# Performance work log

Measured on AMD Instinct MI355X. Metric: run time of the kernel, lower is better.

Reference implementation:

```python
import jax, jax.numpy as jnp
import numpy as np

N_NODES = 20000
N_EDGES = 320000
EMB = 256
K_DIFF = 3
BN_EPS = 1e-5


def conv1d(x, w, b, stride):
    # x: [N, Cin, L], w: [Cout, Cin, K]
    y = jax.lax.conv_general_dilated(x, w, window_strides=(stride,), padding='VALID',
                                     dimension_numbers=('NCH', 'OIH', 'NCH'))
    return y + b[None, :, None]


def batchnorm_train(x, gamma, beta):
    # training-mode BatchNorm1d over (N, L) per channel, biased variance
    m = jnp.mean(x, axis=(0, 2), keepdims=True)
    v = jnp.var(x, axis=(0, 2), keepdims=True)
    return (x - m) * jax.lax.rsqrt(v + BN_EPS) * gamma[None, :, None] + beta[None, :, None]


def dconv(X, W, b, row, col, norm_out, norm_in, n):
    # Diffusion convolution (pytorch_geometric_temporal DConv), K hops,
    # forward (out-degree) and backward (in-degree) random walks.
    def prop(x, norm):
        msg = norm[:, None] * x[row]                    # [E, F] gather
        return jax.ops.segment_sum(msg, col, num_segments=n)  # scatter-add to targets

    K = W.shape[1]
    Tx_0 = X
    Tx_1 = X
    H = X @ W[0, 0] + X @ W[1, 0]
    if K > 1:
        Tx_1_o = prop(X, norm_out)
        Tx_1_i = prop(X, norm_in)
        H = H + Tx_1_o @ W[0, 1] + Tx_1_i @ W[1, 1]
    for k in range(2, K):
        Tx_2_o = 2.0 * prop(Tx_1_o, norm_out) - Tx_0
        Tx_2_i = 2.0 * prop(Tx_1_i, norm_in) - Tx_0
        H = H + Tx_2_o @ W[0, k] + Tx_2_i @ W[1, k]
        Tx_0, Tx_1_o, Tx_1_i = Tx_1, Tx_2_o, Tx_2_i
    return H + b


def setup_inputs() -> dict:
    key = jax.random.key(0)
    ks = jax.random.split(key, 16)
    d_in = 2 * EMB  # concat([X, H])
    inp = {
        'x': jax.random.normal(ks[0], (N_NODES, 1, 100), dtype=jnp.float32),
        'edge_index': jax.random.randint(ks[1], (2, N_EDGES), 0, N_NODES, dtype=jnp.int32),
        'hidden_state': jax.random.normal(ks[2], (N_NODES, EMB), dtype=jnp.float32),
        'conv1_w': jax.random.normal(ks[3], (32, 1, 10), dtype=jnp.float32) * 0.2,
        'conv1_b': jnp.zeros((32,), jnp.float32),
        'bn1_gamma': jnp.ones((32,), jnp.float32),
        'bn1_beta': jnp.zeros((32,), jnp.float32),
        'conv2_w': jax.random.normal(ks[4], (32, 32, 10), dtype=jnp.float32) * 0.05,
        'conv2_b': jnp.zeros((32,), jnp.float32),
        'bn2_gamma': jnp.ones((32,), jnp.float32),
        'bn2_beta': jnp.zeros((32,), jnp.float32),
        'W_z': jax.random.normal(ks[5], (2, K_DIFF, d_in, EMB), dtype=jnp.float32) * 0.05,
        'b_z': jnp.zeros((EMB,), jnp.float32),
        'W_r': jax.random.normal(ks[6], (2, K_DIFF, d_in, EMB), dtype=jnp.float32) * 0.05,
        'b_r': jnp.zeros((EMB,), jnp.float32),
        'W_h': jax.random.normal(ks[7], (2, K_DIFF, d_in, EMB), dtype=jnp.float32) * 0.05,
        'b_h': jnp.zeros((EMB,), jnp.float32),
    }
    return inp


def reference(x, edge_index, hidden_state, conv1_w, conv1_b, bn1_gamma, bn1_beta,
              conv2_w, conv2_b, bn2_gamma, bn2_beta, W_z, b_z, W_r, b_r, W_h, b_h):
    n = x.shape[0]
    # CNN embedding: conv -> relu -> bn, twice
    h = batchnorm_train(jax.nn.relu(conv1d(x, conv1_w, conv1_b, 3)), bn1_gamma, bn1_beta)
    h = batchnorm_train(jax.nn.relu(conv1d(h, conv2_w, conv2_b, 3)), bn2_gamma, bn2_beta)
    X = h.reshape(n, -1)  # [N, EMB]

    row, col = edge_index[0], edge_index[1]
    ones = jnp.ones((row.shape[0],), X.dtype)
    deg_out = jax.ops.segment_sum(ones, row, num_segments=n)
    deg_in = jax.ops.segment_sum(ones, col, num_segments=n)
    norm_out = (1.0 / deg_out)[row]
    norm_in = (1.0 / deg_in)[col]

    H0 = hidden_state
    XH = jnp.concatenate([X, H0], axis=1)
    Z = jax.nn.sigmoid(dconv(XH, W_z, b_z, row, col, norm_out, norm_in, n))
    R = jax.nn.sigmoid(dconv(XH, W_r, b_r, row, col, norm_out, norm_in, n))
    XRH = jnp.concatenate([X, R * H0], axis=1)
    H_tilde = jnp.tanh(dconv(XRH, W_h, b_h, row, col, norm_out, norm_in, n))
    H = Z * H0 + (1.0 - Z) * H_tilde
    return jax.nn.relu(H)
```

## Files before the change

### kernel.cpp

```cpp
#include <hip/hip_runtime.h>
#include <cstdint>
#include <cstddef>

#define NN 20000
#define NE 320000
#define SBUF 10240000

typedef float f32x4 __attribute__((ext_vector_type(4)));
typedef short s16x8 __attribute__((ext_vector_type(8)));
typedef unsigned short us;

__device__ __forceinline__ us f2bf(float x){
    unsigned u = __float_as_uint(x);
    unsigned r = (u + 0x7fffu + ((u >> 16) & 1u)) >> 16;
    return (us)r;
}
__device__ __forceinline__ float bf2f(us s){
    return __uint_as_float(((unsigned)s) << 16);
}

__device__ __forceinline__ void gl16(const void* g, void* l){
    __builtin_amdgcn_global_load_lds((const __attribute__((address_space(1))) unsigned int*)g,
                                     (__attribute__((address_space(3))) unsigned int*)l, 16, 0, 0);
}

__device__ __forceinline__ void upd8(uint4 v, float w, float* ao, float* ai){
    float f0=__uint_as_float(v.x<<16), f1=__uint_as_float(v.x&0xffff0000u);
    float f2=__uint_as_float(v.y<<16), f3=__uint_as_float(v.y&0xffff0000u);
    float f4=__uint_as_float(v.z<<16), f5=__uint_as_float(v.z&0xffff0000u);
    float f6=__uint_as_float(v.w<<16), f7=__uint_as_float(v.w&0xffff0000u);
    ao[0]=fmaf(w,f0,ao[0]); ao[1]=fmaf(w,f1,ao[1]); ao[2]=fmaf(w,f2,ao[2]); ao[3]=fmaf(w,f3,ao[3]);
    ao[4]=fmaf(w,f4,ao[4]); ao[5]=fmaf(w,f5,ao[5]); ao[6]=fmaf(w,f6,ao[6]); ao[7]=fmaf(w,f7,ao[7]);
    ai[0]+=f0; ai[1]+=f1; ai[2]+=f2; ai[3]+=f3; ai[4]+=f4; ai[5]+=f5; ai[6]+=f6; ai[7]+=f7;
}
__device__ __forceinline__ void updw(uint4 v, float w, float* a){
    float f0=__uint_as_float(v.x<<16), f1=__uint_as_float(v.x&0xffff0000u);
    float f2=__uint_as_float(v.y<<16), f3=__uint_as_float(v.y&0xffff0000u);
    float f4=__uint_as_float(v.z<<16), f5=__uint_as_float(v.z&0xffff0000u);
    float f6=__uint_as_float(v.w<<16), f7=__uint_as_float(v.w&0xffff0000u);
    a[0]=fmaf(w,f0,a[0]); a[1]=fmaf(w,f1,a[1]); a[2]=fmaf(w,f2,a[2]); a[3]=fmaf(w,f3,a[3]);
    a[4]=fmaf(w,f4,a[4]); a[5]=fmaf(w,f5,a[5]); a[6]=fmaf(w,f6,a[6]); a[7]=fmaf(w,f7,a[7]);
}
__device__ __forceinline__ uint4 pack8(const float* a){
    uint4 r;
    r.x=((unsigned)f2bf(a[1])<<16)|f2bf(a[0]);
    r.y=((unsigned)f2bf(a[3])<<16)|f2bf(a[2]);
    r.z=((unsigned)f2bf(a[5])<<16)|f2bf(a[4]);
    r.w=((unsigned)f2bf(a[7])<<16)|f2bf(a[6]);
    return r;
}
__device__ __forceinline__ uint4 pack8s(const float* a, float s){
    uint4 r;
    r.x=((unsigned)f2bf(s*a[1])<<16)|f2bf(s*a[0]);
    r.y=((unsigned)f2bf(s*a[3])<<16)|f2bf(s*a[2]);
    r.z=((unsigned)f2bf(s*a[5])<<16)|f2bf(s*a[4]);
    r.w=((unsigned)f2bf(s*a[7])<<16)|f2bf(s*a[6]);
    return r;
}


__global__ void k_zero(uint32_t* p, int n){
    int i = blockIdx.x*256 + threadIdx.x;
    if(i < n) p[i] = 0u;
}

__global__ void k_degree(const int* __restrict__ ei, int* degout, int* degin){
    int e = blockIdx.x*256 + threadIdx.x;
    if(e < NE){
        atomicAdd(&degout[ei[e]], 1);
        atomicAdd(&degin[ei[NE+e]], 1);
    }
}

__global__ void k_scan(const int* __restrict__ degin, int* __restrict__ coloff,
                       float* __restrict__ invdegin){
    __shared__ int part[1024];
    int t = threadIdx.x;
    int base = t*20;
    int s = 0;
    for(int k=0;k<20;k++){ int i = base+k; if(i < NN) s += degin[i]; }
    part[t] = s;
    __syncthreads();
    for(int off=1; off<1024; off<<=1){
        int v = (t>=off) ? part[t-off] : 0;
        __syncthreads();
        part[t] += v;
        __syncthreads();
    }
    int run = (t>0) ? part[t-1] : 0;
    for(int k=0;k<20;k++){
        int i = base+k;
        if(i < NN){
            int d = degin[i];
            coloff[i] = run;
            run += d;
            invdegin[i] = (d>0) ? (1.0f/(float)d) : 0.0f;
        }
    }
    if(t==1023) coloff[NN] = part[1023];
}

__global__ void k_csr(const int* __restrict__ ei, const int* __restrict__ degout,
                      const int* __restrict__ coloff, int* cnt, int2* __restrict__ ew){
    int e = blockIdx.x*256 + threadIdx.x;
    if(e < NE){
        int r = ei[e], c = ei[NE+e];
        int pos = coloff[c] + atomicAdd(&cnt[c], 1);
        int2 v; v.x = r; v.y = __float_as_int(1.0f/(float)degout[r]);
        ew[pos] = v;
    }
}


__global__ void k_conv1(const float* __restrict__ x, const float* __restrict__ w1,
                        const float* __restrict__ b1, us* __restrict__ y1T){
    __shared__ float w[320];
    __shared__ float bb[32];
    int t = threadIdx.x;
    for(int i=t;i<320;i+=256) w[i] = w1[i];
    if(t < 32) bb[t] = b1[t];
    __syncthreads();
    int gid = blockIdx.x*256 + t;
    int node = gid>>5, p = gid&31;
    us* yo = y1T + (size_t)node*1024 + p*32;
    if(p >= 31){
        uint4 z = {0,0,0,0};
        *(uint4*)yo = z; *(uint4*)(yo+8) = z;
        *(uint4*)(yo+16) = z; *(uint4*)(yo+24) = z;
        return;
    }
    const float* xr = x + node*100 + 3*p;
    float xv[10];
    #pragma unroll
    for(int k=0;k<10;k++) xv[k] = xr[k];
    float o[32];
    #pragma unroll
    for(int c=0;c<32;c++){
        float a = bb[c];
        #pragma unroll
        for(int k=0;k<10;k++) a = fmaf(w[c*10+k], xv[k], a);
        o[c] = fmaxf(a, 0.0f);
    }
    *(uint4*)yo      = pack8(o);
    *(uint4*)(yo+8)  = pack8(o+8);
    *(uint4*)(yo+16) = pack8(o+16);
    *(uint4*)(yo+24) = pack8(o+24);
}

__global__ void k_chanstats_T(const us* __restrict__ y, float* __restrict__ sq){
    int tid = blockIdx.x*256 + threadIdx.x;
    int slot = tid & 1023;
    int c = slot & 31;
    int node0 = tid >> 10;
    float s = 0.f, q = 0.f;
    for(int n=node0; n<NN; n+=64){
        float v = bf2f(y[(size_t)n*1024 + slot]);
        s += v; q = fmaf(v, v, q);
    }
    s += __shfl_xor(s, 32);
    q += __shfl_xor(q, 32);
    if((threadIdx.x & 63) < 32){
        atomicAdd(&sq[c], s);
        atomicAdd(&sq[32+c], q);
    }
}

template<int SLOTS, int PPC>
__global__ void k_chanstats_bf(const us* __restrict__ y, float* __restrict__ sq){
    int tid = blockIdx.x*blockDim.x + threadIdx.x;
    int slot = tid & (SLOTS-1);
    int node0 = tid / SLOTS;
    int nstride = (gridDim.x*blockDim.x) / SLOTS;
    int c = slot / PPC;
    float s = 0.f, q = 0.f;
    for(int n=node0; n<NN; n+=nstride){
        float v = bf2f(y[(size_t)n*SLOTS + slot]);
        s += v; q = fmaf(v, v, q);
    }
    #pragma unroll
    for(int m=PPC>>1; m>0; m>>=1){
        s += __shfl_xor(s, m);
        q += __shfl_xor(q, m);
    }
    if((threadIdx.x & (PPC-1)) == 0){
        atomicAdd(&sq[c], s);
        atomicAdd(&sq[32+c], q);
    }
}

__global__ void k_bnfin(const float* __restrict__ sq, const float* __restrict__ gamma,
                        const float* __restrict__ beta, float* __restrict__ scsh,
                        float inv_count){
    int c = threadIdx.x;
    if(c < 32){
        float m = sq[c]*inv_count;
        float v = sq[32+c]*inv_count - m*m;
        float sc = gamma[c]*rsqrtf(v + 1e-5f);
        scsh[c] = sc;
        scsh[32+c] = beta[c] - m*sc;
    }
}

__global__ void k_wfold(const float* __restrict__ w2, const float* __restrict__ scsh1,
                        us* __restrict__ Bf){
    int idx = blockIdx.x*256 + threadIdx.x;
    if(idx >= 10240) return;
    int kk = idx >> 10, c2 = (idx >> 5) & 31, c = idx & 31;
    Bf[idx] = f2bf(scsh1[c] * w2[c2*320 + c*10 + kk]);
}

__global__ void k_wbias(const float* __restrict__ w2, const float* __restrict__ scsh1,
                        const float* __restrict__ b2, float* __restrict__ biasc){
    int t = threadIdx.x;
    int c2 = t >> 3, part = t & 7;
    float s = 0.f;
    for(int i=part; i<320; i+=8)
        s += scsh1[32 + i/10] * w2[c2*320 + i];
    s += __shfl_xor(s,1); s += __shfl_xor(s,2); s += __shfl_xor(s,4);
    if(part == 0) biasc[c2] = b2[c2] + s;
}

__global__ void __launch_bounds__(256) k_conv2m(const us* __restrict__ y1T,
        const us* __restrict__ Bf, const float* __restrict__ biasc,
        us* __restrict__ Xpre){
    int t = threadIdx.x;
    int wv = t>>6, l = t&63;
    int l15 = l&15, g = l>>4;
    int r0 = blockIdx.x*64 + wv*16;
    int arow = r0 + l15;
    int an = arow>>3, ap = arow&7;
    const us* abase = y1T + (size_t)an*1024 + (3*ap)*32 + g*8;
    const us* bbase = Bf + (size_t)l15*32 + g*8;
    f32x4 acc0 = {}, acc1 = {};
    #pragma unroll
    for(int kk=0;kk<10;kk++){
        s16x8 af = *(const s16x8*)(abase + kk*32);
        s16x8 b0 = *(const s16x8*)(bbase + kk*1024);
        s16x8 b1 = *(const s16x8*)(bbase + kk*1024 + 512);
        acc0 = __builtin_amdgcn_mfma_f32_16x16x32_bf16(af, b0, acc0, 0, 0, 0);
        acc1 = __builtin_amdgcn_mfma_f32_16x16x32_bf16(af, b1, acc1, 0, 0, 0);
    }
    int base = r0 + g*4;
    int n = base>>3, p0 = base&7;
    #pragma unroll
    for(int nf=0;nf<2;nf++){
        int c2 = nf*16 + l15;
        float bb = biasc[c2];
        f32x4 a = nf ? acc1 : acc0;
        float v0 = fmaxf(a[0]+bb,0.f), v1 = fmaxf(a[1]+bb,0.f);
        float v2 = fmaxf(a[2]+bb,0.f), v3 = fmaxf(a[3]+bb,0.f);
        uint2 pk;
        pk.x = ((unsigned)f2bf(v1)<<16)|f2bf(v0);
        pk.y = ((unsigned)f2bf(v3)<<16)|f2bf(v2);
        *(uint2*)&Xpre[(size_t)n*256 + c2*8 + p0] = pk;
    }
}

__global__ void __launch_bounds__(256) k_prep(const us* __restrict__ Xpre,
        const float* __restrict__ scsh, const float* __restrict__ h0,
        us* __restrict__ XHp){
    int node = blockIdx.x*4 + (threadIdx.x>>6);
    if(node >= NN) return;
    int lane = threadIdx.x & 63;
    int half = lane>>5, g = lane&31;
    uint4 o;
    if(half == 0){
        uint4 v = *(const uint4*)(Xpre + (size_t)node*256 + g*8);
        float sc = scsh[g], sh = scsh[32+g];
        float y[8];
        y[0]=fmaf(sc,__uint_as_float(v.x<<16),sh); y[1]=fmaf(sc,__uint_as_float(v.x&0xffff0000u),sh);
        y[2]=fmaf(sc,__uint_as_float(v.y<<16),sh); y[3]=fmaf(sc,__uint_as_float(v.y&0xffff0000u),sh);
        y[4]=fmaf(sc,__uint_as_float(v.z<<16),sh); y[5]=fmaf(sc,__uint_as_float(v.z&0xffff0000u),sh);
        y[6]=fmaf(sc,__uint_as_float(v.w<<16),sh); y[7]=fmaf(sc,__uint_as_float(v.w&0xffff0000u),sh);
        o = pack8(y);
    }else{
        float4 a = *(const float4*)(h0 + (size_t)node*256 + g*8);
        float4 b = *(const float4*)(h0 + (size_t)node*256 + g*8 + 4);
        float y[8] = {a.x,a.y,a.z,a.w,b.x,b.y,b.z,b.w};
        o = pack8(y);
    }
    *(uint4*)(XHp + (size_t)node*512 + (size_t)g*16 + half*8) = o;
}


__device__ __forceinline__ float weff_val(const float* W, int term, size_t base){
    const size_t S = 512*256;
    if(term==0)      return W[0*S+base] + W[3*S+base] - W[2*S+base] - W[5*S+base];
    else if(term==1) return W[1*S+base];
    else if(term==2) return W[4*S+base];
    else if(term==3) return 2.0f*W[2*S+base];
    else             return 2.0f*W[5*S+base];
}

__global__ void k_weff_zr_t(const float* __restrict__ Wz, const float* __restrict__ Wr,
                            us* __restrict__ Wt){
    int k = blockIdx.x*256 + threadIdx.x;
    int col = blockIdx.y;
    const float* W = (col < 256) ? Wz : Wr;
    int j = col & 255;
    int kb = k >> 8, rr = k & 255;
    size_t base = (size_t)((kb & 1)*256 + rr)*256 + j;
    Wt[(size_t)col*2560 + k] = f2bf(weff_val(W, kb>>1, base));
}

__global__ void k_weff_h_t(const float* __restrict__ Wh, us* __restrict__ Wt){
    int k = blockIdx.x*256 + threadIdx.x;
    int col = blockIdx.y;
    int kb = k >> 8, rr = k & 255;
    size_t base = (size_t)((kb & 1)*256 + rr)*256 + col;
    Wt[(size_t)col*2560 + k] = f2bf(weff_val(Wh, kb>>1, base));
}


__global__ void __launch_bounds__(256) k_prop1(const us* __restrict__ XHp,
        const int* __restrict__ coloff, const int2* __restrict__ ew,
        const float* __restrict__ invdeg, us* __restrict__ T1op, us* __restrict__ T1ip){
    int node = blockIdx.x*4 + (threadIdx.x>>6);
    if(node >= NN) return;
    int lane = threadIdx.x & 63;
    size_t lo = (size_t)(lane&31)*16 + (lane>>5)*8;
    int s = __builtin_amdgcn_readfirstlane(coloff[node]);
    int e = __builtin_amdgcn_readfirstlane(coloff[node+1]);
    float ao[8]={0,0,0,0,0,0,0,0}, ai[8]={0,0,0,0,0,0,0,0};
    int j = s;
    for(; j+7 < e; j += 8){
        int2 ed[8]; uint4 v[8];
        #pragma unroll
        for(int i=0;i<8;i++) ed[i] = ew[j+i];
        #pragma unroll
        for(int i=0;i<8;i++) v[i] = *(const uint4*)(XHp+(size_t)ed[i].x*512+lo);
        #pragma unroll
        for(int i=0;i<8;i++) upd8(v[i], __int_as_float(ed[i].y), ao, ai);
    }
    for(; j < e; j++){
        int2 ed = ew[j];
        uint4 v = *(const uint4*)(XHp+(size_t)ed.x*512+lo);
        upd8(v, __int_as_float(ed.y), ao, ai);
    }
    float wi = invdeg[node];
    *(uint4*)(T1op+(size_t)node*512+lo) = pack8(ao);
    *(uint4*)(T1ip+(size_t)node*512+lo) = pack8s(ai,wi);
}

__global__ void __launch_bounds__(256) k_prop2(const us* __restrict__ T1op,
        const us* __restrict__ T1ip,
        const int* __restrict__ coloff, const int2* __restrict__ ew,
        const float* __restrict__ invdeg, us* __restrict__ P2op, us* __restrict__ P2ip){
    int node = blockIdx.x*4 + (threadIdx.x>>6);
    if(node >= NN) return;
    int lane = threadIdx.x & 63;
    size_t lo = (size_t)(lane&31)*16 + (lane>>5)*8;
    int s = __builtin_amdgcn_readfirstlane(coloff[node]);
    int e = __builtin_amdgcn_readfirstlane(coloff[node+1]);
    float ao[8]={0,0,0,0,0,0,0,0}, ai[8]={0,0,0,0,0,0,0,0};
    int j = s;
    for(; j+3 < e; j += 4){
        int2 ed[4]; uint4 va[4], vb[4];
        #pragma unroll
        for(int i=0;i<4;i++) ed[i] = ew[j+i];
        #pragma unroll
        for(int i=0;i<4;i++){
            size_t o = (size_t)ed[i].x*512+lo;
            va[i] = *(const uint4*)(T1op+o);
            vb[i] = *(const uint4*)(T1ip+o);
        }
        #pragma unroll
        for(int i=0;i<4;i++){
            updw(va[i], __int_as_float(ed[i].y), ao);
            updw(vb[i], 1.0f, ai);
        }
    }
    for(; j < e; j++){
        int2 ed = ew[j];
        size_t o = (size_t)ed.x*512+lo;
        updw(*(const uint4*)(T1op+o), __int_as_float(ed.y), ao);
        updw(*(const uint4*)(T1ip+o), 1.0f, ai);
    }
    float wi = invdeg[node];
    *(uint4*)(P2op+(size_t)node*512+lo) = pack8(ao);
    *(uint4*)(P2ip+(size_t)node*512+lo) = pack8s(ai,wi);
}

__global__ void __launch_bounds__(256) k_propu(const us* __restrict__ Yin,
        const int* __restrict__ coloff, const int2* __restrict__ ew,
        const float* __restrict__ invdeg, us* __restrict__ Pout){
    int node = blockIdx.x*4 + (threadIdx.x>>6);
    if(node >= NN) return;
    int lane = threadIdx.x & 63;
    int half = lane>>5;
    size_t lo = (size_t)(lane&31)*16 + half*8;
    int s = __builtin_amdgcn_readfirstlane(coloff[node]);
    int e = __builtin_amdgcn_readfirstlane(coloff[node+1]);
    float a[8]={0,0,0,0,0,0,0,0};
    int j = s;
    for(; j+7 < e; j += 8){
        int2 ed[8]; uint4 v[8];
        #pragma unroll
        for(int i=0;i<8;i++) ed[i] = ew[j+i];
        #pragma unroll
        for(int i=0;i<8;i++) v[i] = *(const uint4*)(Yin+(size_t)ed[i].x*512+lo);
        #pragma unroll
        for(int i=0;i<8;i++) updw(v[i], half ? 1.0f : __int_as_float(ed[i].y), a);
    }
    for(; j < e; j++){
        int2 ed = ew[j];
        uint4 v = *(const uint4*)(Yin+(size_t)ed.x*512+lo);
        updw(v, half ? 1.0f : __int_as_float(ed.y), a);
    }
    float sc = half ? invdeg[node] : 1.0f;
    *(uint4*)(Pout+(size_t)node*512+lo) = pack8s(a,sc);
}


template<int MODE, int BNT>
__global__ void __launch_bounds__(256) k_gemm(const us* __restrict__ XG,
        const us* __restrict__ RG, const us* __restrict__ Wt,
        const float* __restrict__ bias0, const float* __restrict__ bias1,
        const float* __restrict__ h0, const float* __restrict__ Zin,
        float* __restrict__ out0, us* __restrict__ out1){
    constexpr int WN = BNT/32;
    constexpr int NB = BNT/64;
    __shared__ us As[2][4096];
    __shared__ us Bs[2][BNT*32];
    int t = threadIdx.x;
    int wid = t >> 6, lane = t & 63;
    int l15 = lane & 15, kg = lane >> 4;

    int bid = blockIdx.x;
    int xcd = bid & 7, sblk = bid >> 3;
    int cidx = sblk & 3, r = (sblk >> 2)*8 + xcd;
    if(r >= 157) return;
    int row0 = r*128, col0 = cidx*BNT;
    int rowbase = (wid >> 1)*64, colbase = (wid & 1)*(BNT/2);
    int swz = (l15 >> 1) & 3;

    int srA[2], sgA[2];
    size_t rowoffA[2];
    #pragma unroll
    for(int i=0;i<2;i++){
        int c = t + i*256;
        srA[i] = c >> 2;
        sgA[i] = (c & 3) ^ ((srA[i] >> 1) & 3);
        int gr = row0 + srA[i];
        gr = (gr < NN) ? gr : NN-1;
        rowoffA[i] = (size_t)gr*512 + (size_t)sgA[i]*16;
    }
    int srB[NB], sgB[NB];
    size_t coloffB[NB];
    #pragma unroll
    for(int i=0;i<NB;i++){
        int c = t + i*256;
        srB[i] = c >> 2;
        sgB[i] = (c & 3) ^ ((srB[i] >> 1) & 3);
        coloffB[i] = (size_t)(col0+srB[i])*2560 + (size_t)sgB[i]*8;
    }

    f32x4 acc[4][WN] = {};

    auto stage = [&](int buf, int s){
        int kb = s >> 3;
        int ktc = (s & 7) * 4;
        const us* Ap;
        if(MODE == 0){
            Ap = XG + (size_t)(kb >> 1) * SBUF + (size_t)(kb & 1) * 8;
        }else{
            if((kb & 1) == 0) Ap = XG + (size_t)(kb >> 1) * SBUF;
            else Ap = RG + (size_t)((kb + 1) >> 2) * SBUF + (size_t)(((kb + 1) >> 1) & 1) * 8;
        }
        #pragma unroll
        for(int i=0;i<2;i++)
            gl16(Ap + rowoffA[i] + (size_t)ktc*16, &As[buf][(t+i*256)*8]);
        const us* Wp = Wt + (size_t)kb*256 + (s & 7)*32;
        #pragma unroll
        for(int i=0;i<NB;i++)
            gl16(Wp + coloffB[i], &Bs[buf][(t+i*256)*8]);
    };

    stage(0, 0);
    stage(1, 1);
    for(int step=0; step<80; ++step){
        int cur = step & 1;
        if(step < 79){
            if(MODE == 0) asm volatile("s_waitcnt vmcnt(4)" ::: "memory");
            else          asm volatile("s_waitcnt vmcnt(3)" ::: "memory");
        }else{
            asm volatile("s_waitcnt vmcnt(0)" ::: "memory");
        }
        __builtin_amdgcn_s_barrier();
        s16x8 af[4], bfr[WN];
        #pragma unroll
        for(int i=0;i<4;i++){
            int row = rowbase + i*16 + l15;
            af[i] = *(const s16x8*)&As[cur][(row*4 + (kg ^ swz))*8];
        }
        #pragma unroll
        for(int n=0;n<WN;n++){
            int colr = colbase + n*16 + l15;
            bfr[n] = *(const s16x8*)&Bs[cur][(colr*4 + (kg ^ swz))*8];
        }
        asm volatile("s_waitcnt lgkmcnt(0)" ::: "memory");
        __builtin_amdgcn_sched_barrier(0);
        __builtin_amdgcn_s_barrier();
        if(step < 78) stage(cur, step+2);
        __builtin_amdgcn_s_setprio(1);
        #pragma unroll
        for(int mi=0;mi<4;mi++){
            #pragma unroll
            for(int ni=0;ni<WN;ni++){
                acc[mi][ni] = __builtin_amdgcn_mfma_f32_16x16x32_bf16(
                    af[mi], bfr[ni], acc[mi][ni], 0, 0, 0);
            }
        }
        __builtin_amdgcn_s_setprio(0);
    }

    #pragma unroll
    for(int mi=0;mi<4;mi++){
        int gr0 = row0 + rowbase + mi*16 + kg*4;
        #pragma unroll
        for(int ni=0;ni<WN;ni++){
            int j = col0 + colbase + ni*16 + l15;
            #pragma unroll
            for(int rr=0;rr<4;rr++){
                int gr = gr0 + rr;
                if(gr < NN){
                    float a = acc[mi][ni][rr];
                    if(MODE == 0){
                        if(j < 256){
                            out0[(size_t)gr*256 + j] = 1.0f/(1.0f + expf(-(a + bias0[j])));
                        }else{
                            int jj = j - 256;
                            float rv = 1.0f/(1.0f + expf(-(a + bias1[jj])));
                            us v = f2bf(rv * h0[(size_t)gr*256 + jj]);
                            size_t base = (size_t)gr*512 + (size_t)(jj>>3)*16 + (jj&7);
                            out1[base] = v;
                            out1[base+8] = v;
                        }
                    }else{
                        float z = Zin[(size_t)gr*256 + j];
                        float ht = tanhf(a + bias0[j]);
                        float H = z*h0[(size_t)gr*256 + j] + (1.0f - z)*ht;
                        out0[(size_t)gr*256 + j] = fmaxf(H, 0.0f);
                    }
                }
            }
        }
    }
}


extern "C" void kernel_launch(void* const* d_in, const int* in_sizes, int n_in,
                              void* d_out, int out_size, void* d_ws, size_t ws_size,
                              hipStream_t stream){
    const float* x   = (const float*)d_in[0];
    const int*   ei  = (const int*)  d_in[1];
    const float* h0  = (const float*)d_in[2];
    const float* w1  = (const float*)d_in[3];
    const float* b1  = (const float*)d_in[4];
    const float* g1  = (const float*)d_in[5];
    const float* be1 = (const float*)d_in[6];
    const float* w2  = (const float*)d_in[7];
    const float* b2  = (const float*)d_in[8];
    const float* g2  = (const float*)d_in[9];
    const float* be2 = (const float*)d_in[10];
    const float* Wz  = (const float*)d_in[11];
    const float* bz  = (const float*)d_in[12];
    const float* Wr  = (const float*)d_in[13];
    const float* br  = (const float*)d_in[14];
    const float* Wh  = (const float*)d_in[15];
    const float* bh  = (const float*)d_in[16];
    float* out = (float*)d_out;
    float* wsf = (float*)d_ws;
    (void)in_sizes; (void)n_in; (void)out_size;

    const size_t O_DEGO=0, O_DEGI=20000, O_CNT=40000, O_BN=60000;
    const size_t O_COLOFF=60288, O_EW=80384, O_INVDEG=720384;
    const size_t O_WTZR=740480, O_WTH=1395840;
    const size_t O_XPRE=1723520;
    const size_t O_XG=4283520;
    const size_t O_RG=29883520;
    const size_t O_Z=45243520;
    const size_t O_BF=50363520;
    const size_t WS_NEED_BYTES = (size_t)50366080 * 4;
    if(ws_size < WS_NEED_BYTES) return;

    const size_t SW = 5120000;

    int* degout = (int*)(wsf + O_DEGO);
    int* degin  = (int*)(wsf + O_DEGI);
    int* cnt    = (int*)(wsf + O_CNT);
    float* bn   = wsf + O_BN;
    int* coloff = (int*)(wsf + O_COLOFF);
    int2* ew    = (int2*)(wsf + O_EW);
    float* invdeg = wsf + O_INVDEG;
    us* Wtzr = (us*)(wsf + O_WTZR);
    us* Wth  = (us*)(wsf + O_WTH);
    us* Xpre = (us*)(wsf + O_XPRE);
    us* XG   = (us*)(wsf + O_XG);
    us* RG   = (us*)(wsf + O_RG);
    us* XHp  = XG;
    us* T1op = (us*)(wsf + O_XG + SW);
    us* T1ip = (us*)(wsf + O_XG + 2*SW);
    us* P2op = (us*)(wsf + O_XG + 3*SW);
    us* P2ip = (us*)(wsf + O_XG + 4*SW);
    us* RHp  = RG;
    us* Q1p  = (us*)(wsf + O_RG + SW);
    us* Q2p  = (us*)(wsf + O_RG + 2*SW);
    float* Z = wsf + O_Z;
    us* Bf   = (us*)(wsf + O_BF);
    us* y1T  = T1op;

    k_zero<<<236,256,0,stream>>>((uint32_t*)(wsf + O_DEGO), 60256);
    k_degree<<<1250,256,0,stream>>>(ei, degout, degin);
    k_scan<<<1,1024,0,stream>>>(degin, coloff, invdeg);
    k_csr<<<1250,256,0,stream>>>(ei, degout, coloff, cnt, ew);

    k_conv1<<<2500,256,0,stream>>>(x, w1, b1, y1T);
    k_chanstats_T<<<256,256,0,stream>>>(y1T, bn+0);
    k_bnfin<<<1,32,0,stream>>>(bn+0, g1, be1, bn+64, 1.0f/620000.0f);
    k_wfold<<<40,256,0,stream>>>(w2, bn+64, Bf);
    k_wbias<<<1,256,0,stream>>>(w2, bn+64, b2, bn+256);
    k_conv2m<<<2500,256,0,stream>>>(y1T, Bf, bn+256, Xpre);
    k_chanstats_bf<256,8><<<64,256,0,stream>>>(Xpre, bn+128);
    k_bnfin<<<1,32,0,stream>>>(bn+128, g2, be2, bn+192, 1.0f/160000.0f);
    k_prep<<<5000,256,0,stream>>>(Xpre, bn+192, h0, XHp);

    k_weff_zr_t<<<dim3(10,512),256,0,stream>>>(Wz, Wr, Wtzr);
    k_weff_h_t<<<dim3(10,256),256,0,stream>>>(Wh, Wth);

    k_prop1<<<5000,256,0,stream>>>(XHp, coloff, ew, invdeg, T1op, T1ip);
    k_prop2<<<5000,256,0,stream>>>(T1op, T1ip, coloff, ew, invdeg, P2op, P2ip);

    k_gemm<0,128><<<640,256,0,stream>>>(XG, RG, Wtzr, bz, br, h0, nullptr, Z, RHp);

    k_propu<<<5000,256,0,stream>>>(RHp, coloff, ew, invdeg, Q1p);
    k_propu<<<5000,256,0,stream>>>(Q1p, coloff, ew, invdeg, Q2p);

    k_gemm<1,64><<<640,256,0,stream>>>(XG, RG, Wth, bh, nullptr, h0, Z, out, nullptr);
}
```

Before: 732.1 us.

## Triple-buffer GEMM shared tiles and transpose weight folding through LDS

The GEMM main loop moves from double to triple buffering of the A/B shared-memory tiles. This lets it drop the second barrier and the lgkmcnt wait before issuing the next async global-to-LDS stage, so loads overlap more with MFMA work. The cost is more LDS per block, which may lower occupancy. Separately, the effective-weight folding kernels now stage a 64x64 tile through padded shared memory, so both reads and the transposed bf16 writes are coalesced instead of strided.

```diff
diff --git a/kernel.cpp b/kernel.cpp
--- a/kernel.cpp
+++ b/kernel.cpp
@@ -292,23 +292,35 @@
     else             return 2.0f*W[5*S+base];
 }
 
-__global__ void k_weff_zr_t(const float* __restrict__ Wz, const float* __restrict__ Wr,
-                            us* __restrict__ Wt){
-    int k = blockIdx.x*256 + threadIdx.x;
-    int col = blockIdx.y;
-    const float* W = (col < 256) ? Wz : Wr;
-    int j = col & 255;
-    int kb = k >> 8, rr = k & 255;
-    size_t base = (size_t)((kb & 1)*256 + rr)*256 + j;
-    Wt[(size_t)col*2560 + k] = f2bf(weff_val(W, kb>>1, base));
-}
-
-__global__ void k_weff_h_t(const float* __restrict__ Wh, us* __restrict__ Wt){
-    int k = blockIdx.x*256 + threadIdx.x;
-    int col = blockIdx.y;
-    int kb = k >> 8, rr = k & 255;
-    size_t base = (size_t)((kb & 1)*256 + rr)*256 + col;
-    Wt[(size_t)col*2560 + k] = f2bf(weff_val(Wh, kb>>1, base));
+template<int NCOL>
+__global__ void __launch_bounds__(256) k_wefft(const float* __restrict__ Wa,
+        const float* __restrict__ Wb, us* __restrict__ Wt){
+    __shared__ float tile[64*65];
+    int bx = blockIdx.x;
+    constexpr int CT = NCOL/64;
+    int kb = bx / (CT*4);
+    int rem = bx % (CT*4);
+    int ct = rem >> 2, rt = rem & 3;
+    int col0 = ct*64, rr0 = rt*64;
+    const float* W = (col0 < 256) ? Wa : Wb;
+    int jb = col0 & 255;
+    int term = kb >> 1, half = kb & 1;
+    int t = threadIdx.x;
+    int j_l = t & 63, r4 = t >> 6;
+    #pragma unroll
+    for(int it=0; it<16; it++){
+        int rr_l = it*4 + r4;
+        int row = half*256 + rr0 + rr_l;
+        size_t base = (size_t)row*256 + jb + j_l;
+        tile[j_l*65 + rr_l] = weff_val(W, term, base);
+    }
+    __syncthreads();
+    int rr_w = t & 63;
+    #pragma unroll
+    for(int it=0; it<16; it++){
+        int col_l = it*4 + r4;
+        Wt[(size_t)(col0+col_l)*2560 + kb*256 + rr0 + rr_w] = f2bf(tile[col_l*65 + rr_w]);
+    }
 }
 
 
@@ -420,8 +432,8 @@
         float* __restrict__ out0, us* __restrict__ out1){
     constexpr int WN = BNT/32;
     constexpr int NB = BNT/64;
-    __shared__ us As[2][4096];
-    __shared__ us Bs[2][BNT*32];
+    __shared__ us As[3][4096];
+    __shared__ us Bs[3][BNT*32];
     int t = threadIdx.x;
     int wid = t >> 6, lane = t & 63;
     int l15 = lane & 15, kg = lane >> 4;
@@ -478,8 +490,8 @@
 
     stage(0, 0);
     stage(1, 1);
+    int cur = 0;
     for(int step=0; step<80; ++step){
-        int cur = step & 1;
         if(step < 79){
             if(MODE == 0) asm volatile("s_waitcnt vmcnt(4)" ::: "memory");
             else          asm volatile("s_waitcnt vmcnt(3)" ::: "memory");
@@ -487,6 +499,7 @@
             asm volatile("s_waitcnt vmcnt(0)" ::: "memory");
         }
         __builtin_amdgcn_s_barrier();
+        __builtin_amdgcn_sched_barrier(0);
         s16x8 af[4], bfr[WN];
         #pragma unroll
         for(int i=0;i<4;i++){
@@ -498,10 +511,10 @@
             int colr = colbase + n*16 + l15;
             bfr[n] = *(const s16x8*)&Bs[cur][(colr*4 + (kg ^ swz))*8];
         }
-        asm volatile("s_waitcnt lgkmcnt(0)" ::: "memory");
-        __builtin_amdgcn_sched_barrier(0);
-        __builtin_amdgcn_s_barrier();
-        if(step < 78) stage(cur, step+2);
+        if(step < 78){
+            int nxt = cur + 2; if(nxt >= 3) nxt -= 3;
+            stage(nxt, step+2);
+        }
         __builtin_amdgcn_s_setprio(1);
         #pragma unroll
         for(int mi=0;mi<4;mi++){
@@ -512,6 +525,7 @@
             }
         }
         __builtin_amdgcn_s_setprio(0);
+        cur = (cur == 2) ? 0 : cur + 1;
     }
 
     #pragma unroll
@@ -625,8 +639,8 @@
     k_bnfin<<<1,32,0,stream>>>(bn+128, g2, be2, bn+192, 1.0f/160000.0f);
     k_prep<<<5000,256,0,stream>>>(Xpre, bn+192, h0, XHp);
 
-    k_weff_zr_t<<<dim3(10,512),256,0,stream>>>(Wz, Wr, Wtzr);
-    k_weff_h_t<<<dim3(10,256),256,0,stream>>>(Wh, Wth);
+    k_wefft<512><<<320,256,0,stream>>>(Wz, Wr, Wtzr);
+    k_wefft<256><<<160,256,0,stream>>>(Wh, Wh, Wth);
 
     k_prop1<<<5000,256,0,stream>>>(XHp, coloff, ew, invdeg, T1op, T1ip);
     k_prop2<<<5000,256,0,stream>>>(T1op, T1ip, coloff, ew, invdeg, P2op, P2ip);
```

Measured after the change: 734.7 us. Within noise of the previous version (+0.4%).
